# Kernel optimization log

Measured on AMD Instinct MI355X. Metric: run time of the kernel, lower is better.

The kernel has to match this reference:

```python
import jax, jax.numpy as jnp
import numpy as np

B, S, IN, OUT = 4, 2048, 4096, 4096

def setup_inputs() -> dict:
    key = jax.random.key(0)
    k1, k2, k3, k4 = jax.random.split(key, 4)
    x = jax.random.normal(k1, (B, S, IN), dtype=jnp.float32)
    # sign is mathematically +/-1 (sign of original fp weights)
    sign = jnp.sign(jax.random.normal(k2, (OUT, IN), dtype=jnp.float32))
    # per-row scale = mean(|W|), strictly positive
    scale = jax.random.uniform(k3, (OUT,), dtype=jnp.float32, minval=1e-3, maxval=0.1)
    bias = jax.random.normal(k4, (OUT,), dtype=jnp.float32)
    return {"x": x, "sign": sign, "scale": scale, "bias": bias}

def reference(x, sign, scale, bias) -> jnp.ndarray:
    # y = (x @ sign.T) * scale + bias  -- W approx diag(scale) * sign(W_orig)
    y = jnp.einsum('bsi,oi->bso', x, sign)
    return y * scale + bias
```

## Files before the change

kernel.cpp:

```cpp
#include <hip/hip_runtime.h>

#define M_DIM 8192
#define N_DIM 4096
#define K_DIM 4096
#define BK 32
#define NT 128

typedef __attribute__((ext_vector_type(8))) short bf16x8;
typedef __attribute__((ext_vector_type(8))) unsigned short u16x8;
typedef __attribute__((ext_vector_type(16))) float f32x16;

__device__ inline unsigned short f32_to_bf16_rne(float f) {
  unsigned int u = __float_as_uint(f);
  u += 0x7FFFu + ((u >> 16) & 1u);
  return (unsigned short)(u >> 16);
}

__global__ __launch_bounds__(256) void cvt_f32_bf16_kernel(
    const float* __restrict__ in, unsigned short* __restrict__ out) {
  const int i = (blockIdx.x * 256 + threadIdx.x) * 8;
  float4 v0 = *(const float4*)(in + i);
  float4 v1 = *(const float4*)(in + i + 4);
  u16x8 o;
  o[0] = f32_to_bf16_rne(v0.x);
  o[1] = f32_to_bf16_rne(v0.y);
  o[2] = f32_to_bf16_rne(v0.z);
  o[3] = f32_to_bf16_rne(v0.w);
  o[4] = f32_to_bf16_rne(v1.x);
  o[5] = f32_to_bf16_rne(v1.y);
  o[6] = f32_to_bf16_rne(v1.z);
  o[7] = f32_to_bf16_rne(v1.w);
  *(u16x8*)(out + i) = o;
}

__device__ inline void gld_lds16(const void* g, void* l) {
  __builtin_amdgcn_global_load_lds(
      (const __attribute__((address_space(1))) void*)(g),
      (__attribute__((address_space(3))) void*)(l), 16, 0, 0);
}

__global__ __launch_bounds__(512, 2) void gemm_sign_kernel(
    const unsigned short* __restrict__ A,
    const unsigned short* __restrict__ Bm,
    const float* __restrict__ scale,
    const float* __restrict__ bias,
    float* __restrict__ C) {
  __shared__ __align__(16) unsigned char sm[131072];

  const int tid   = threadIdx.x;
  const int lane  = tid & 63;
  const int wave  = tid >> 6;
  const int waveM = wave >> 2;
  const int waveN = wave & 3;
  const int l31   = lane & 31;
  const int hi    = lane >> 5;

  const int bid   = blockIdx.x;
  const int wgid  = (bid & 7) * 64 + (bid >> 3);
  const int mBase = (wgid >> 4) * 256;
  const int nBase = (wgid & 15) * 256;

  const int srow = tid >> 2;
  const int gcol = ((tid & 3) ^ ((tid >> 3) & 3) ^ ((tid >> 5) & 3)) * 8;
  const unsigned short* aP = A  + (size_t)(mBase + srow) * K_DIM + gcol;
  const unsigned short* bP = Bm + (size_t)(nBase + srow) * K_DIM + gcol;
  const size_t rowStr128 = (size_t)128 * K_DIM;

#define STAGE(SBUF) do {                                                \
    gld_lds16(aP,             sm + (SBUF)*16384 + tid*16);              \
    gld_lds16(aP + rowStr128, sm + (SBUF)*16384 + 8192 + tid*16);       \
    gld_lds16(bP,             sm + 65536 + (SBUF)*16384 + tid*16);      \
    gld_lds16(bP + rowStr128, sm + 65536 + (SBUF)*16384 + 8192 + tid*16); \
    aP += BK; bP += BK;                                                 \
  } while (0)

  const int p = ((l31 >> 1) & 3) ^ ((l31 >> 3) & 3);
  const unsigned char* aRd0 = &sm[(waveM * 128 + l31) * 64 + ((hi ^ p) * 16)];
  const unsigned char* aRd1 = &sm[(waveM * 128 + l31) * 64 + (((2 + hi) ^ p) * 16)];
  const unsigned char* bRd0 = &sm[65536 + (waveN * 64 + l31) * 64 + ((hi ^ p) * 16)];
  const unsigned char* bRd1 = &sm[65536 + (waveN * 64 + l31) * 64 + (((2 + hi) ^ p) * 16)];

  f32x16 acc[4][2];
#pragma unroll
  for (int i = 0; i < 4; ++i)
#pragma unroll
    for (int j = 0; j < 2; ++j)
#pragma unroll
      for (int r = 0; r < 16; ++r)
        acc[i][j][r] = 0.f;

#define BODY(BUF, DO_STAGE, SBUF, VMODE)                                \
  {                                                                     \
    bf16x8 af[4][2], bf[2][2];                                          \
    _Pragma("unroll")                                                   \
    for (int mi = 0; mi < 4; ++mi) {                                    \
      af[mi][0] = *(const bf16x8*)(aRd0 + (BUF) * 16384 + mi * 2048);   \
      af[mi][1] = *(const bf16x8*)(aRd1 + (BUF) * 16384 + mi * 2048);   \
    }                                                                   \
    _Pragma("unroll")                                                   \
    for (int ni = 0; ni < 2; ++ni) {                                    \
      bf[ni][0] = *(const bf16x8*)(bRd0 + (BUF) * 16384 + ni * 2048);   \
      bf[ni][1] = *(const bf16x8*)(bRd1 + (BUF) * 16384 + ni * 2048);   \
    }                                                                   \
    if (DO_STAGE) STAGE(SBUF);                                          \
    if ((VMODE) == 1) asm volatile("s_waitcnt vmcnt(4)" ::: "memory");  \
    if ((VMODE) == 2) asm volatile("s_waitcnt vmcnt(0)" ::: "memory");  \
    __builtin_amdgcn_s_barrier();                                       \
    asm volatile("s_waitcnt lgkmcnt(0)" ::: "memory");                  \
    __builtin_amdgcn_s_setprio(1);                                      \
    _Pragma("unroll")                                                   \
    for (int mi = 0; mi < 4; ++mi)                                      \
      _Pragma("unroll")                                                 \
      for (int ni = 0; ni < 2; ++ni) {                                  \
        acc[mi][ni] = __builtin_amdgcn_mfma_f32_32x32x16_bf16(          \
            af[mi][0], bf[ni][0], acc[mi][ni], 0, 0, 0);                \
        acc[mi][ni] = __builtin_amdgcn_mfma_f32_32x32x16_bf16(          \
            af[mi][1], bf[ni][1], acc[mi][ni], 0, 0, 0);                \
      }                                                                 \
    __builtin_amdgcn_s_setprio(0);                                      \
    __builtin_amdgcn_s_barrier();                                       \
  }

  STAGE(0); STAGE(1); STAGE(2);
  asm volatile("s_waitcnt vmcnt(4)" ::: "memory");
  __builtin_amdgcn_s_barrier();

  for (int it = 0; it < 31; ++it) {
    BODY(0, 1, 3, 1);
    BODY(1, 1, 0, 1);
    BODY(2, 1, 1, 1);
    BODY(3, 1, 2, 1);
  }

  BODY(0, 1, 3, 1);
  BODY(1, 0, 0, 2);
  BODY(2, 0, 0, 0);
  BODY(3, 0, 0, 0);

#undef BODY
#undef STAGE

#pragma unroll
  for (int ni = 0; ni < 2; ++ni) {
    const int c = nBase + waveN * 64 + ni * 32 + l31;
    const float sc = scale[c];
    const float bs = bias[c];
#pragma unroll
    for (int mi = 0; mi < 4; ++mi) {
      const int r0 = mBase + waveM * 128 + mi * 32 + 4 * hi;
#pragma unroll
      for (int r = 0; r < 16; ++r) {
        const int row = r0 + (r & 3) + 8 * (r >> 2);
        C[(size_t)row * N_DIM + c] = acc[mi][ni][r] * sc + bs;
      }
    }
  }
}

extern "C" void kernel_launch(void* const* d_in, const int* in_sizes, int n_in,
                              void* d_out, int out_size, void* d_ws, size_t ws_size,
                              hipStream_t stream) {
  const float* x     = (const float*)d_in[0];
  const float* sign  = (const float*)d_in[1];
  const float* scale = (const float*)d_in[2];
  const float* bias  = (const float*)d_in[3];
  float* out = (float*)d_out;

  unsigned short* xb    = (unsigned short*)d_ws;
  unsigned short* signb = xb + (size_t)M_DIM * K_DIM;

  cvt_f32_bf16_kernel<<<(M_DIM * K_DIM) / 2048, 256, 0, stream>>>(x, xb);
  cvt_f32_bf16_kernel<<<(N_DIM * K_DIM) / 2048, 256, 0, stream>>>(sign, signb);

  gemm_sign_kernel<<<dim3(512), dim3(512), 0, stream>>>(xb, signb, scale, bias, out);
}
```

Measured before the change: 515.9 us.

## Split each K-step into two MFMA phases and interleave A/B tile staging

Each K-step is split into two half-phases covering the upper and lower M sub-tiles. The global-to-LDS prefetch for the A tile is issued in the first phase and the B tile in the second, which spreads memory issue across the compute. The wait is relaxed from vmcnt(4) to vmcnt(8), so two prefetch stages can stay in flight instead of one. Fewer A fragments are live at once, but barriers per K-step double from two to four, which adds synchronisation overhead.

```diff
diff --git a/kernel.cpp b/kernel.cpp
--- a/kernel.cpp
+++ b/kernel.cpp
@@ -66,12 +66,15 @@
   const unsigned short* bP = Bm + (size_t)(nBase + srow) * K_DIM + gcol;
   const size_t rowStr128 = (size_t)128 * K_DIM;
 
-#define STAGE(SBUF) do {                                                \
+#define STAGE_A(SBUF) do {                                              \
     gld_lds16(aP,             sm + (SBUF)*16384 + tid*16);              \
     gld_lds16(aP + rowStr128, sm + (SBUF)*16384 + 8192 + tid*16);       \
+    aP += BK;                                                           \
+  } while (0)
+#define STAGE_B(SBUF) do {                                              \
     gld_lds16(bP,             sm + 65536 + (SBUF)*16384 + tid*16);      \
     gld_lds16(bP + rowStr128, sm + 65536 + (SBUF)*16384 + 8192 + tid*16); \
-    aP += BK; bP += BK;                                                 \
+    bP += BK;                                                           \
   } while (0)
 
   const int p = ((l31 >> 1) & 3) ^ ((l31 >> 3) & 3);
@@ -89,56 +92,85 @@
       for (int r = 0; r < 16; ++r)
         acc[i][j][r] = 0.f;
 
-#define BODY(BUF, DO_STAGE, SBUF, VMODE)                                \
+#define BODY(BUF, DO_STAGE, VMODE)                                      \
   {                                                                     \
-    bf16x8 af[4][2], bf[2][2];                                          \
-    _Pragma("unroll")                                                   \
-    for (int mi = 0; mi < 4; ++mi) {                                    \
-      af[mi][0] = *(const bf16x8*)(aRd0 + (BUF) * 16384 + mi * 2048);   \
-      af[mi][1] = *(const bf16x8*)(aRd1 + (BUF) * 16384 + mi * 2048);   \
+    bf16x8 bf[2][2];                                                    \
+    {                                                                   \
+      bf16x8 af[2][2];                                                  \
+      _Pragma("unroll")                                                 \
+      for (int mi = 0; mi < 2; ++mi) {                                  \
+        af[mi][0] = *(const bf16x8*)(aRd0 + (BUF) * 16384 + mi * 2048); \
+        af[mi][1] = *(const bf16x8*)(aRd1 + (BUF) * 16384 + mi * 2048); \
+      }                                                                 \
+      _Pragma("unroll")                                                 \
+      for (int ni = 0; ni < 2; ++ni) {                                  \
+        bf[ni][0] = *(const bf16x8*)(bRd0 + (BUF) * 16384 + ni * 2048); \
+        bf[ni][1] = *(const bf16x8*)(bRd1 + (BUF) * 16384 + ni * 2048); \
+      }                                                                 \
+      if (DO_STAGE) STAGE_A((BUF + 3) & 3);                             \
+      __builtin_amdgcn_s_barrier();                                     \
+      asm volatile("s_waitcnt lgkmcnt(0)" ::: "memory");                \
+      __builtin_amdgcn_s_setprio(1);                                    \
+      _Pragma("unroll")                                                 \
+      for (int mi = 0; mi < 2; ++mi)                                    \
+        _Pragma("unroll")                                               \
+        for (int ni = 0; ni < 2; ++ni) {                                \
+          acc[mi][ni] = __builtin_amdgcn_mfma_f32_32x32x16_bf16(        \
+              af[mi][0], bf[ni][0], acc[mi][ni], 0, 0, 0);              \
+          acc[mi][ni] = __builtin_amdgcn_mfma_f32_32x32x16_bf16(        \
+              af[mi][1], bf[ni][1], acc[mi][ni], 0, 0, 0);              \
+        }                                                               \
+      __builtin_amdgcn_s_setprio(0);                                    \
+      __builtin_amdgcn_s_barrier();                                     \
     }                                                                   \
-    _Pragma("unroll")                                                   \
-    for (int ni = 0; ni < 2; ++ni) {                                    \
-      bf[ni][0] = *(const bf16x8*)(bRd0 + (BUF) * 16384 + ni * 2048);   \
-      bf[ni][1] = *(const bf16x8*)(bRd1 + (BUF) * 16384 + ni * 2048);   \
+    {                                                                   \
+      bf16x8 af[2][2];                                                  \
+      _Pragma("unroll")                                                 \
+      for (int mi = 0; mi < 2; ++mi) {                                  \
+        af[mi][0] = *(const bf16x8*)(aRd0 + (BUF) * 16384 + (2 + mi) * 2048); \
+        af[mi][1] = *(const bf16x8*)(aRd1 + (BUF) * 16384 + (2 + mi) * 2048); \
+      }                                                                 \
+      if (DO_STAGE) STAGE_B((BUF + 3) & 3);                             \
+      if ((VMODE) == 1) asm volatile("s_waitcnt vmcnt(8)" ::: "memory"); \
+      if ((VMODE) == 2) asm volatile("s_waitcnt vmcnt(0)" ::: "memory"); \
+      __builtin_amdgcn_s_barrier();                                     \
+      asm volatile("s_waitcnt lgkmcnt(0)" ::: "memory");                \
+      __builtin_amdgcn_s_setprio(1);                                    \
+      _Pragma("unroll")                                                 \
+      for (int mi = 0; mi < 2; ++mi)                                    \
+        _Pragma("unroll")                                               \
+        for (int ni = 0; ni < 2; ++ni) {                                \
+          acc[2 + mi][ni] = __builtin_amdgcn_mfma_f32_32x32x16_bf16(    \
+              af[mi][0], bf[ni][0], acc[2 + mi][ni], 0, 0, 0);          \
+          acc[2 + mi][ni] = __builtin_amdgcn_mfma_f32_32x32x16_bf16(    \
+              af[mi][1], bf[ni][1], acc[2 + mi][ni], 0, 0, 0);          \
+        }                                                               \
+      __builtin_amdgcn_s_setprio(0);                                    \
+      __builtin_amdgcn_s_barrier();                                     \
     }                                                                   \
-    if (DO_STAGE) STAGE(SBUF);                                          \
-    if ((VMODE) == 1) asm volatile("s_waitcnt vmcnt(4)" ::: "memory");  \
-    if ((VMODE) == 2) asm volatile("s_waitcnt vmcnt(0)" ::: "memory");  \
-    __builtin_amdgcn_s_barrier();                                       \
-    asm volatile("s_waitcnt lgkmcnt(0)" ::: "memory");                  \
-    __builtin_amdgcn_s_setprio(1);                                      \
-    _Pragma("unroll")                                                   \
-    for (int mi = 0; mi < 4; ++mi)                                      \
-      _Pragma("unroll")                                                 \
-      for (int ni = 0; ni < 2; ++ni) {                                  \
-        acc[mi][ni] = __builtin_amdgcn_mfma_f32_32x32x16_bf16(          \
-            af[mi][0], bf[ni][0], acc[mi][ni], 0, 0, 0);                \
-        acc[mi][ni] = __builtin_amdgcn_mfma_f32_32x32x16_bf16(          \
-            af[mi][1], bf[ni][1], acc[mi][ni], 0, 0, 0);                \
-      }                                                                 \
-    __builtin_amdgcn_s_setprio(0);                                      \
-    __builtin_amdgcn_s_barrier();                                       \
   }
 
-  STAGE(0); STAGE(1); STAGE(2);
-  asm volatile("s_waitcnt vmcnt(4)" ::: "memory");
+  STAGE_A(0); STAGE_B(0);
+  STAGE_A(1); STAGE_B(1);
+  STAGE_A(2); STAGE_B(2);
+  asm volatile("s_waitcnt vmcnt(8)" ::: "memory");
   __builtin_amdgcn_s_barrier();
 
   for (int it = 0; it < 31; ++it) {
-    BODY(0, 1, 3, 1);
-    BODY(1, 1, 0, 1);
-    BODY(2, 1, 1, 1);
-    BODY(3, 1, 2, 1);
+    BODY(0, 1, 1);
+    BODY(1, 1, 1);
+    BODY(2, 1, 1);
+    BODY(3, 1, 1);
   }
 
-  BODY(0, 1, 3, 1);
-  BODY(1, 0, 0, 2);
-  BODY(2, 0, 0, 0);
-  BODY(3, 0, 0, 0);
+  BODY(0, 1, 1);
+  BODY(1, 0, 2);
+  BODY(2, 0, 0);
+  BODY(3, 0, 0);
 
 #undef BODY
-#undef STAGE
+#undef STAGE_A
+#undef STAGE_B
 
 #pragma unroll
   for (int ni = 0; ni < 2; ++ni) {
```

After: 494.2 us. 1.04x faster.
